# Kernel optimization log

Hardware: AMD Instinct MI355X
Metric: run time of the kernel (lower is better)

The kernel has to match this reference:

```python
import jax, jax.numpy as jnp
import numpy as np

NUM_EMBEDDINGS = 1024
EMBEDDING_DIM = 64
SCALE = 1.0 / NUM_EMBEDDINGS


def setup_inputs() -> dict:
    key = jax.random.key(0)
    k1, k2 = jax.random.split(key)
    input = jax.random.normal(k1, (16, EMBEDDING_DIM, 64, 64), dtype=jnp.float32)
    # nn.Embedding weight initialized uniform(-scale, scale)
    codebook = jax.random.uniform(k2, (NUM_EMBEDDINGS, EMBEDDING_DIM),
                                  dtype=jnp.float32, minval=-SCALE, maxval=SCALE)
    return {"input": input, "codebook": codebook}


def reference(input, codebook):
    # NCHW -> NHWC, flatten spatial+batch to tokens [N, D]
    x = jnp.transpose(input, (0, 2, 3, 1))           # [B, H, W, D]
    B, H, W, D = x.shape
    flat = x.reshape(-1, D)                          # [N, D]
    dists = (jnp.sum(flat ** 2, axis=1, keepdims=True)
             + jnp.sum(codebook ** 2, axis=1)
             - 2.0 * flat @ codebook.T)              # [N, K]
    idx = jnp.argmin(dists, axis=-1).reshape(B, H, W)  # [B, H, W]
    quantized = codebook[idx]                        # [B, H, W, D]
    return jnp.transpose(quantized, (0, 3, 1, 2))    # [B, D, H, W]
```

## Files before the change

### kernel.cpp

```cpp
#include <hip/hip_runtime.h>

typedef short short8 __attribute__((ext_vector_type(8)));
typedef float f32x4 __attribute__((ext_vector_type(4)));
typedef unsigned long long u64;

#define NE 1024
#define D 64
#define HW 4096
#define MARGIN 3.0e-3f
#define FLT_MAX_F 3.402823466e+38f
#define MSTRIDE 17

#define WS_BN  0
#define WS_EBF 4096

__device__ __forceinline__ unsigned short f2bf(float f) {
    unsigned u = __float_as_uint(f);
    return (unsigned short)((u + 0x7fffu + ((u >> 16) & 1u)) >> 16);
}

__device__ __forceinline__ float np_sum64_sq(const float* v) {
    float s[8];
#pragma unroll
    for (int j = 0; j < 8; ++j) s[j] = __fmul_rn(v[j], v[j]);
#pragma unroll
    for (int i = 8; i < 64; i += 8) {
#pragma unroll
        for (int j = 0; j < 8; ++j)
            s[j] = __fadd_rn(s[j], __fmul_rn(v[i + j], v[i + j]));
    }
    return __fadd_rn(__fadd_rn(__fadd_rn(s[0], s[1]), __fadd_rn(s[2], s[3])),
                     __fadd_rn(__fadd_rn(s[4], s[5]), __fadd_rn(s[6], s[7])));
}

__global__ __launch_bounds__(256) void kP_prep(
        const float* __restrict__ cb, float* __restrict__ bn,
        unsigned short* __restrict__ ebf) {
    const int gid = blockIdx.x * 256 + threadIdx.x;
    ebf[gid] = f2bf(cb[gid]);
    if (gid < NE) {
        float row[D];
        const float4* r4 = reinterpret_cast<const float4*>(cb + (size_t)gid * D);
#pragma unroll
        for (int i = 0; i < 16; ++i) {
            float4 v = r4[i];
            row[4*i+0] = v.x; row[4*i+1] = v.y; row[4*i+2] = v.z; row[4*i+3] = v.w;
        }
        bn[gid] = np_sum64_sq(row);
    }
}

__global__ __launch_bounds__(512, 2) void k_mega(
        const float* __restrict__ in, const unsigned short* __restrict__ ebf,
        const float* __restrict__ bn_g, const float* __restrict__ cb,
        float* __restrict__ out) {
    __shared__ unsigned short ebq[2 * 128 * 64];
    __shared__ float sbn[NE];
    __shared__ u64 lmask[128 * MSTRIDE];
    __shared__ unsigned short win_s[128];

    const int tid  = threadIdx.x;
    const int lane = tid & 63, w = tid >> 6;
    const int lcol = lane & 15, lhi = lane >> 4, lrow = lhi * 4;
    const int tokw = blockIdx.x * 128 + w * 16;
    const int b = tokw >> 12, hwb = tokw & 4095;

#pragma unroll
    for (int i = 0; i < 2; ++i)
        sbn[tid + i * 512] = __fmul_rn(-0.5f, bn_g[tid + i * 512]);

    const float* xbase = in + (size_t)b * (D * HW);
    const int hw0 = hwb + lcol;
    const int kb = lhi * 8;
    short8 B00, B01;
    {
        const float* p;
        p = xbase + (size_t)kb * HW + hw0;
#pragma unroll
        for (int j = 0; j < 8; ++j) B00[j] = (short)f2bf(p[(size_t)j * HW]);
        p = xbase + (size_t)(kb + 32) * HW + hw0;
#pragma unroll
        for (int j = 0; j < 8; ++j) B01[j] = (short)f2bf(p[(size_t)j * HW]);
    }

    const int swz   = (lcol & 7) << 4;
    const int aoff0 = lcol * 128 + ((lhi * 16) ^ swz);
    const int aoff1 = lcol * 128 + ((64 + lhi * 16) ^ swz);

    int4 pf0, pf1;
#define LOADC(C) { const int4* s_ = (const int4*)(ebf + (size_t)(C) * 8192);  \
                   pf0 = s_[tid]; pf1 = s_[tid + 512]; }
#define WRITEC(BUF) { int4 t_[2] = {pf0, pf1};                                \
    _Pragma("unroll")                                                         \
    for (int i = 0; i < 2; ++i) {                                             \
        int L = (tid + i * 512) * 16;                                         \
        int row = L >> 7, wi = L & 127;                                       \
        *(int4*)((char*)ebq + (BUF) * 16384 + row * 128                       \
                 + (wi ^ ((row & 7) << 4))) = t_[i];                          \
    } }

#define CHUNK_MFMA(BUF, C, CT)                                                \
    const char* lp = (const char*)ebq + (BUF) * 16384 + (CT) * 2048;          \
    short8 A0 = *(const short8*)(lp + aoff0);                                 \
    short8 A1 = *(const short8*)(lp + aoff1);                                 \
    f32x4 acc = *(const f32x4*)(sbn + (C) * 128 + (CT) * 16 + lrow);          \
    acc = __builtin_amdgcn_mfma_f32_16x16x32_bf16(A0, B00, acc, 0, 0, 0);     \
    acc = __builtin_amdgcn_mfma_f32_16x16x32_bf16(A1, B01, acc, 0, 0, 0);

    f32x4 vA = {-FLT_MAX_F, -FLT_MAX_F, -FLT_MAX_F, -FLT_MAX_F};
    LOADC(0)
    WRITEC(0)
    __syncthreads();
    for (int c = 0; c < 8; ++c) {
        const int buf = c & 1;
        if (c < 7) LOADC(c + 1)
#pragma unroll
        for (int ct = 0; ct < 8; ++ct) {
            CHUNK_MFMA(buf, c, ct)
#pragma unroll
            for (int r = 0; r < 4; ++r) vA[r] = fmaxf(vA[r], acc[r]);
        }
        if (c < 7) WRITEC(buf ^ 1)
        __syncthreads();
    }
    float v0 = fmaxf(fmaxf(vA[0], vA[1]), fmaxf(vA[2], vA[3]));
    v0 = fmaxf(v0, __shfl_xor(v0, 16)); v0 = fmaxf(v0, __shfl_xor(v0, 32));
    const float athr = v0 - 0.5f * MARGIN;
    const int tl = w * 16 + lcol;

    LOADC(0)
    WRITEC(0)
    __syncthreads();
    for (int c = 0; c < 8; ++c) {
        const int buf = c & 1;
        if (c < 7) LOADC(c + 1)
        u64 w0 = 0, w1 = 0;
#pragma unroll
        for (int ct = 0; ct < 8; ++ct) {
            CHUNK_MFMA(buf, c, ct)
#pragma unroll
            for (int r = 0; r < 4; ++r) {
                const int bit = (ct & 3) * 16 + lrow + r;
                if (acc[r] >= athr) { if (ct < 4) w0 |= 1ull << bit; else w1 |= 1ull << bit; }
            }
        }
        w0 |= __shfl_xor(w0, 16); w0 |= __shfl_xor(w0, 32);
        w1 |= __shfl_xor(w1, 16); w1 |= __shfl_xor(w1, 32);
        if (lhi == 0) {
            lmask[tl * MSTRIDE + 2 * c]     = w0;
            lmask[tl * MSTRIDE + 2 * c + 1] = w1;
        }
        if (c < 7) WRITEC(buf ^ 1)
        __syncthreads();
    }

    {
        const int tok_l = tid >> 2, sub = tid & 3;
        const int tok = blockIdx.x * 128 + tok_l;
        const int tb = tok >> 12, thw = tok & 4095;
        const float* x = in + (size_t)tb * (D * HW) + thw;
        float xv[D];
#pragma unroll
        for (int d = 0; d < D; ++d) xv[d] = x[(size_t)d * HW];
        const float a = np_sum64_sq(xv);

        u64 best = ~0ull;
        int kp = -1;
        int pos = 0;
        for (int wd = 0; wd < 16; ++wd) {
            u64 m = lmask[tok_l * MSTRIDE + wd];
            while (m) {
                const int k = wd * 64 + (int)__builtin_ctzll(m);
                m &= m - 1;
                if (((pos++) & 3) != sub) continue;
                if (kp < 0) { kp = k; continue; }
                const float* e0 = cb + (size_t)kp * D;
                const float* e1 = cb + (size_t)k * D;
                float d0 = 0.f, d1 = 0.f;
#pragma unroll
                for (int d = 0; d < 64; ++d) {
                    d0 = __fmaf_rn(xv[d], e0[d], d0);
                    d1 = __fmaf_rn(xv[d], e1[d], d1);
                }
                float q0 = __fsub_rn(__fadd_rn(a, bn_g[kp]), __fmul_rn(2.0f, d0));
                float q1 = __fsub_rn(__fadd_rn(a, bn_g[k]),  __fmul_rn(2.0f, d1));
                u64 key0 = (((u64)__float_as_uint(q0)) << 32) | (unsigned)kp;
                u64 key1 = (((u64)__float_as_uint(q1)) << 32) | (unsigned)k;
                u64 kmin = key0 < key1 ? key0 : key1;
                best = best < kmin ? best : kmin;
                kp = -1;
            }
        }
        if (kp >= 0) {
            const float* e0 = cb + (size_t)kp * D;
            float d0 = 0.f;
#pragma unroll
            for (int d = 0; d < 64; ++d) d0 = __fmaf_rn(xv[d], e0[d], d0);
            float q0 = __fsub_rn(__fadd_rn(a, bn_g[kp]), __fmul_rn(2.0f, d0));
            u64 key0 = (((u64)__float_as_uint(q0)) << 32) | (unsigned)kp;
            best = best < key0 ? best : key0;
        }
#pragma unroll
        for (int o = 1; o < 4; o <<= 1) {
            u64 v = __shfl_xor(best, o);
            best = best < v ? best : v;
        }
        if (sub == 0) win_s[tok_l] = (unsigned short)(best & 0x3FFull);
    }
    __syncthreads();

    {
        const int tok_l = tid >> 2, qd = (tid & 3) << 4;
        const int tok = blockIdx.x * 128 + tok_l;
        const int gb = tok >> 12, ghw = tok & 4095;
        const unsigned k = win_s[tok_l];
        const float4* er = reinterpret_cast<const float4*>(cb + (size_t)k * D + qd);
        float* ot = out + (size_t)gb * (D * HW) + ghw;
#pragma unroll
        for (int i = 0; i < 4; ++i) {
            float4 e = er[i];
            ot[(size_t)(qd + 4*i + 0) * HW] = e.x;
            ot[(size_t)(qd + 4*i + 1) * HW] = e.y;
            ot[(size_t)(qd + 4*i + 2) * HW] = e.z;
            ot[(size_t)(qd + 4*i + 3) * HW] = e.w;
        }
    }
}

extern "C" void kernel_launch(void* const* d_in, const int* in_sizes, int n_in,
                              void* d_out, int out_size, void* d_ws, size_t ws_size,
                              hipStream_t stream) {
    const float* in  = (const float*)d_in[0];
    const float* cb  = (const float*)d_in[1];
    float*       out = (float*)d_out;
    char*        ws  = (char*)d_ws;

    float*          bn  = (float*)(ws + WS_BN);
    unsigned short* ebf = (unsigned short*)(ws + WS_EBF);

    hipLaunchKernelGGL(kP_prep, dim3(256), dim3(256), 0, stream, cb, bn, ebf);
    hipLaunchKernelGGL(k_mega,  dim3(512), dim3(512), 0, stream, in, ebf, bn, cb, out);
}
```

Measured before the change: 75.26 us.

## Stage token vectors in LDS and simplify candidate mask packing

The candidate mask is now packed as per-lane 32-bit words written directly to shared memory, replacing 64-bit masks combined with cross-lane shuffles. Each lane's bit layout is decoded back to codebook indices during the rescoring pass. The rescoring stage now loads the block's token vectors once, coalesced, into the reused ebq shared buffer, instead of each thread doing 64 strided global loads into registers. Codebook rows are read as float4. This aims to cut register pressure, shuffles and uncoalesced global traffic, at the cost of an extra barrier and strided LDS reads in the inner loop.

```diff
diff --git a/kernel.cpp b/kernel.cpp
--- a/kernel.cpp
+++ b/kernel.cpp
@@ -9,7 +9,7 @@
 #define HW 4096
 #define MARGIN 3.0e-3f
 #define FLT_MAX_F 3.402823466e+38f
-#define MSTRIDE 17
+#define MST 33
 
 #define WS_BN  0
 #define WS_EBF 4096
@@ -28,6 +28,22 @@
 #pragma unroll
         for (int j = 0; j < 8; ++j)
             s[j] = __fadd_rn(s[j], __fmul_rn(v[i + j], v[i + j]));
+    }
+    return __fadd_rn(__fadd_rn(__fadd_rn(s[0], s[1]), __fadd_rn(s[2], s[3])),
+                     __fadd_rn(__fadd_rn(s[4], s[5]), __fadd_rn(s[6], s[7])));
+}
+
+__device__ __forceinline__ float np_sum64_sq_str(const float* p) {
+    float s[8];
+#pragma unroll
+    for (int j = 0; j < 8; ++j) { float v = p[j * 128]; s[j] = __fmul_rn(v, v); }
+#pragma unroll
+    for (int i = 8; i < 64; i += 8) {
+#pragma unroll
+        for (int j = 0; j < 8; ++j) {
+            float v = p[(i + j) * 128];
+            s[j] = __fadd_rn(s[j], __fmul_rn(v, v));
+        }
     }
     return __fadd_rn(__fadd_rn(__fadd_rn(s[0], s[1]), __fadd_rn(s[2], s[3])),
                      __fadd_rn(__fadd_rn(s[4], s[5]), __fadd_rn(s[6], s[7])));
@@ -56,7 +72,7 @@
         float* __restrict__ out) {
     __shared__ unsigned short ebq[2 * 128 * 64];
     __shared__ float sbn[NE];
-    __shared__ u64 lmask[128 * MSTRIDE];
+    __shared__ unsigned mask32[128 * MST];
     __shared__ unsigned short win_s[128];
 
     const int tid  = threadIdx.x;
@@ -134,53 +150,61 @@
     for (int c = 0; c < 8; ++c) {
         const int buf = c & 1;
         if (c < 7) LOADC(c + 1)
-        u64 w0 = 0, w1 = 0;
+        unsigned m = 0;
 #pragma unroll
         for (int ct = 0; ct < 8; ++ct) {
             CHUNK_MFMA(buf, c, ct)
 #pragma unroll
-            for (int r = 0; r < 4; ++r) {
-                const int bit = (ct & 3) * 16 + lrow + r;
-                if (acc[r] >= athr) { if (ct < 4) w0 |= 1ull << bit; else w1 |= 1ull << bit; }
-            }
-        }
-        w0 |= __shfl_xor(w0, 16); w0 |= __shfl_xor(w0, 32);
-        w1 |= __shfl_xor(w1, 16); w1 |= __shfl_xor(w1, 32);
-        if (lhi == 0) {
-            lmask[tl * MSTRIDE + 2 * c]     = w0;
-            lmask[tl * MSTRIDE + 2 * c + 1] = w1;
-        }
+            for (int r = 0; r < 4; ++r)
+                if (acc[r] >= athr) m |= (1u << (ct * 4 + r));
+        }
+        mask32[tl * MST + c * 4 + lhi] = m;
         if (c < 7) WRITEC(buf ^ 1)
         __syncthreads();
     }
 
+    float* xshare = (float*)ebq;
+    {
+        const int hwb0 = (blockIdx.x * 128) & 4095;
+        const float* xb0 = in + (size_t)((blockIdx.x * 128) >> 12) * (D * HW) + hwb0;
+#pragma unroll
+        for (int i = 0; i < 16; ++i) {
+            const int idx = i * 512 + tid;
+            const int d = idx >> 7, t = idx & 127;
+            xshare[d * 128 + t] = xb0[(size_t)d * HW + t];
+        }
+    }
+    __syncthreads();
+
     {
         const int tok_l = tid >> 2, sub = tid & 3;
-        const int tok = blockIdx.x * 128 + tok_l;
-        const int tb = tok >> 12, thw = tok & 4095;
-        const float* x = in + (size_t)tb * (D * HW) + thw;
-        float xv[D];
-#pragma unroll
-        for (int d = 0; d < D; ++d) xv[d] = x[(size_t)d * HW];
-        const float a = np_sum64_sq(xv);
+        const float* xs = xshare + tok_l;
+        const float a = np_sum64_sq_str(xs);
 
         u64 best = ~0ull;
         int kp = -1;
         int pos = 0;
-        for (int wd = 0; wd < 16; ++wd) {
-            u64 m = lmask[tok_l * MSTRIDE + wd];
+        for (int w32 = 0; w32 < 32; ++w32) {
+            unsigned m = mask32[tok_l * MST + w32];
+            const int kbase = (w32 >> 2) * 128 + (w32 & 3) * 4;
             while (m) {
-                const int k = wd * 64 + (int)__builtin_ctzll(m);
+                const int bit = (int)__builtin_ctz(m);
                 m &= m - 1;
+                const int k = kbase + (bit >> 2) * 16 + (bit & 3);
                 if (((pos++) & 3) != sub) continue;
                 if (kp < 0) { kp = k; continue; }
-                const float* e0 = cb + (size_t)kp * D;
-                const float* e1 = cb + (size_t)k * D;
+                const float4* e0q = reinterpret_cast<const float4*>(cb + (size_t)kp * D);
+                const float4* e1q = reinterpret_cast<const float4*>(cb + (size_t)k * D);
                 float d0 = 0.f, d1 = 0.f;
 #pragma unroll
-                for (int d = 0; d < 64; ++d) {
-                    d0 = __fmaf_rn(xv[d], e0[d], d0);
-                    d1 = __fmaf_rn(xv[d], e1[d], d1);
+                for (int i = 0; i < 16; ++i) {
+                    float4 a4 = e0q[i], b4 = e1q[i];
+                    float x0 = xs[(4*i+0)*128], x1 = xs[(4*i+1)*128];
+                    float x2 = xs[(4*i+2)*128], x3 = xs[(4*i+3)*128];
+                    d0 = __fmaf_rn(x0, a4.x, d0); d0 = __fmaf_rn(x1, a4.y, d0);
+                    d0 = __fmaf_rn(x2, a4.z, d0); d0 = __fmaf_rn(x3, a4.w, d0);
+                    d1 = __fmaf_rn(x0, b4.x, d1); d1 = __fmaf_rn(x1, b4.y, d1);
+                    d1 = __fmaf_rn(x2, b4.z, d1); d1 = __fmaf_rn(x3, b4.w, d1);
                 }
                 float q0 = __fsub_rn(__fadd_rn(a, bn_g[kp]), __fmul_rn(2.0f, d0));
                 float q1 = __fsub_rn(__fadd_rn(a, bn_g[k]),  __fmul_rn(2.0f, d1));
@@ -192,10 +216,16 @@
             }
         }
         if (kp >= 0) {
-            const float* e0 = cb + (size_t)kp * D;
+            const float4* e0q = reinterpret_cast<const float4*>(cb + (size_t)kp * D);
             float d0 = 0.f;
 #pragma unroll
-            for (int d = 0; d < 64; ++d) d0 = __fmaf_rn(xv[d], e0[d], d0);
+            for (int i = 0; i < 16; ++i) {
+                float4 a4 = e0q[i];
+                d0 = __fmaf_rn(xs[(4*i+0)*128], a4.x, d0);
+                d0 = __fmaf_rn(xs[(4*i+1)*128], a4.y, d0);
+                d0 = __fmaf_rn(xs[(4*i+2)*128], a4.z, d0);
+                d0 = __fmaf_rn(xs[(4*i+3)*128], a4.w, d0);
+            }
             float q0 = __fsub_rn(__fadd_rn(a, bn_g[kp]), __fmul_rn(2.0f, d0));
             u64 key0 = (((u64)__float_as_uint(q0)) << 32) | (unsigned)kp;
             best = best < key0 ? best : key0;
```

Result: slower. 80.22 us (+6.6%).
